# Kernel optimization log

Hardware: AMD Instinct MI355X
Metric: run time of the kernel (lower is better)

## Reference

```python
import jax, jax.numpy as jnp
import numpy as np

HEADS = 8
DIM_HEAD = 64
ROPE_BASE = 10000.0


def _rope_rotate(t):
    """lucidrains-style interleaved RoPE on t: [B, H, N, D]."""
    n, d = t.shape[-2], t.shape[-1]
    inv_freq = 1.0 / (ROPE_BASE ** (jnp.arange(0, d, 2, dtype=jnp.float32) / d))  # [D/2]
    freqs = jnp.arange(n, dtype=jnp.float32)[:, None] * inv_freq[None, :]          # [N, D/2]
    freqs = jnp.repeat(freqs, 2, axis=-1)                                           # [N, D], interleaved
    cos = jnp.cos(freqs).astype(t.dtype)
    sin = jnp.sin(freqs).astype(t.dtype)
    # rotate_half with interleaved pairs: (x1, x2) -> (-x2, x1)
    t2 = t.reshape(t.shape[:-1] + (d // 2, 2))
    rot = jnp.stack([-t2[..., 1], t2[..., 0]], axis=-1).reshape(t.shape)
    return t * cos + rot * sin


def setup_inputs() -> dict:
    key = jax.random.key(0)
    k1, k2, k3, k4 = jax.random.split(key, 4)
    B, N, DIM = 8, 1024, 512
    hidden = HEADS * DIM_HEAD  # 512
    x = jax.random.normal(k1, (B, N, DIM), dtype=jnp.float32)
    pos_bias = jax.random.normal(k2, (HEADS, N, N), dtype=jnp.float32) * 0.1
    w_qkv = jax.random.normal(k3, (DIM, hidden * 3), dtype=jnp.float32) * (DIM ** -0.5)
    w_out = jax.random.normal(k4, (hidden, DIM), dtype=jnp.float32) * (hidden ** -0.5)
    return {"x": x, "pos_bias": pos_bias, "w_qkv": w_qkv, "w_out": w_out}


def reference(x, pos_bias, w_qkv, w_out):
    B, N, _ = x.shape
    qkv = x @ w_qkv                                   # [B, N, 3*H*D]
    q, k, v = jnp.split(qkv, 3, axis=-1)

    def split_heads(t):
        return t.reshape(B, N, HEADS, DIM_HEAD).transpose(0, 2, 1, 3)  # [B, H, N, D]

    q, k, v = map(split_heads, (q, k, v))
    q = q * (DIM_HEAD ** -0.5)
    q = _rope_rotate(q)
    k = _rope_rotate(k)
    sim = jnp.einsum('bhid,bhjd->bhij', q, k) + pos_bias  # pos_bias [H,N,N] broadcasts over B
    attn = jax.nn.softmax(sim, axis=-1)                    # max-subtracted softmax (stable)
    out = jnp.einsum('bhij,bhjd->bhid', attn, v)
    out = out.transpose(0, 2, 1, 3).reshape(B, N, HEADS * DIM_HEAD)
    return out @ w_out
```

## Files before the change

### kernel.cpp

```cpp
#include <hip/hip_runtime.h>

#define DEV __device__ __forceinline__

typedef __attribute__((ext_vector_type(8))) short bf16x8;
typedef __attribute__((ext_vector_type(4))) short bf16x4;
typedef __attribute__((ext_vector_type(4))) float f32x4;
typedef __attribute__((ext_vector_type(4))) unsigned int u32x4;

constexpr int Bb = 8;
constexpr int Nn = 1024;
constexpr int DIMm = 512;
constexpr int Hh = 8;
constexpr int Dh = 64;
constexpr int Mm = Bb * Nn;
constexpr float LN10K = 9.210340371976184f;
constexpr float LOG2E = 1.4426950408889634f;

DEV short f2bf(float f) {
  unsigned int u = __float_as_uint(f);
  u += 0x7fffu + ((u >> 16) & 1u);
  return (short)(u >> 16);
}

DEV unsigned int cvtpk(float lo, float hi) {
  unsigned int r;
  asm("v_cvt_pk_bf16_f32 %0, %1, %2" : "=v"(r) : "v"(lo), "v"(hi));
  return r;
}

DEV bf16x8 comb(bf16x4 lo, bf16x4 hi) {
  bf16x8 r;
  r[0] = lo[0]; r[1] = lo[1]; r[2] = lo[2]; r[3] = lo[3];
  r[4] = hi[0]; r[5] = hi[1]; r[6] = hi[2]; r[7] = hi[3];
  return r;
}

DEV f32x4 mfma16(bf16x8 a, bf16x8 b, f32x4 c) {
  return __builtin_amdgcn_mfma_f32_16x16x32_bf16(a, b, c, 0, 0, 0);
}

DEV void gload16(const void* g, void* l) {
  __builtin_amdgcn_global_load_lds(
      (const __attribute__((address_space(1))) void*)g,
      (__attribute__((address_space(3))) void*)l, 16, 0, 0);
}

__global__ void prep_kernel(const float* __restrict__ x, const float* __restrict__ wq,
                            const float* __restrict__ wo, short* __restrict__ x_bf,
                            short* __restrict__ wqkvT, short* __restrict__ woutT,
                            float2* __restrict__ tab) {
  int stride = gridDim.x * blockDim.x;
  int t = blockIdx.x * blockDim.x + threadIdx.x;
  for (int i = t; i < Mm * DIMm / 4; i += stride) {
    float4 v = ((const float4*)x)[i];
    bf16x4 o;
    o[0] = f2bf(v.x); o[1] = f2bf(v.y); o[2] = f2bf(v.z); o[3] = f2bf(v.w);
    *(bf16x4*)(x_bf + (size_t)i * 4) = o;
  }
  for (int i = t; i < 1536 * 512; i += stride) {
    int n = i >> 9, k = i & 511;
    wqkvT[i] = f2bf(wq[(size_t)k * 1536 + n]);
  }
  for (int i = t; i < 512 * 512; i += stride) {
    int n = i >> 9, k = i & 511;
    woutT[i] = f2bf(wo[(size_t)k * 512 + n]);
  }
  for (int i = t; i < Nn * 32; i += stride) {
    int n = i >> 5, d2 = i & 31;
    float fr = (float)n * __expf(-(float)(2 * d2) * (LN10K / 64.f));
    float sn, cs;
    __sincosf(fr, &sn, &cs);
    tab[i] = make_float2(cs, sn);
  }
}

template <int QKV>
__global__ __launch_bounds__(256) void gemm_k(const short* __restrict__ A,
                                              const short* __restrict__ Bt,
                                              float* __restrict__ outF,
                                              short* __restrict__ qr,
                                              short* __restrict__ kr,
                                              short* __restrict__ vt,
                                              const float2* __restrict__ tab) {
  __shared__ short Al[128][40];
  __shared__ short Bl[128][40];
  const int tid = threadIdx.x;
  const int lane = tid & 63;
  const int wid = tid >> 6;
  const int wm = wid >> 1, wn = wid & 1;
  const int li = lane & 15, g4 = (lane >> 4) << 2;
  const int m0 = blockIdx.x * 128, n0 = blockIdx.y * 128;

  f32x4 zero4 = {0.f, 0.f, 0.f, 0.f};
  f32x4 acc[4][4];
#pragma unroll
  for (int i = 0; i < 4; ++i)
#pragma unroll
    for (int j = 0; j < 4; ++j) acc[i][j] = zero4;

  for (int kt = 0; kt < 512; kt += 32) {
#pragma unroll
    for (int p = 0; p < 2; ++p) {
      int e = (tid + p * 256) * 8;
      int r = e >> 5, c = e & 31;
      *(u32x4*)(&Al[r][c]) = *(const u32x4*)(A + (size_t)(m0 + r) * 512 + kt + c);
      *(u32x4*)(&Bl[r][c]) = *(const u32x4*)(Bt + (size_t)(n0 + r) * 512 + kt + c);
    }
    __syncthreads();
    bf16x8 af[4], bfr[4];
#pragma unroll
    for (int mt = 0; mt < 4; ++mt) {
      int row = wm * 64 + mt * 16 + li;
      af[mt] = comb(*(const bf16x4*)(&Al[row][g4]), *(const bf16x4*)(&Al[row][16 + g4]));
    }
#pragma unroll
    for (int nt = 0; nt < 4; ++nt) {
      int row = wn * 64 + nt * 16 + li;
      bfr[nt] = comb(*(const bf16x4*)(&Bl[row][g4]), *(const bf16x4*)(&Bl[row][16 + g4]));
    }
#pragma unroll
    for (int mt = 0; mt < 4; ++mt)
#pragma unroll
      for (int nt = 0; nt < 4; ++nt)
        acc[mt][nt] = mfma16(af[mt], bfr[nt], acc[mt][nt]);
    __syncthreads();
  }

  if (QKV == 0) {
#pragma unroll
    for (int mt = 0; mt < 4; ++mt) {
      int mb = m0 + wm * 64 + mt * 16 + g4;
#pragma unroll
      for (int nt = 0; nt < 4; ++nt) {
        int c = n0 + wn * 64 + nt * 16 + li;
#pragma unroll
        for (int r = 0; r < 4; ++r) outF[(size_t)(mb + r) * 512 + c] = acc[mt][nt][r];
      }
    }
  } else {
    const int sec = n0 >> 9;
#pragma unroll
    for (int mt = 0; mt < 4; ++mt) {
      int mb = m0 + wm * 64 + mt * 16 + g4;
      int b_ = mb >> 10;
      int nb = mb & 1023;
#pragma unroll
      for (int nt = 0; nt < 4; ++nt) {
        int c = n0 + wn * 64 + nt * 16 + li;
        int cs = c & 511;
        int hh = cs >> 6, d = cs & 63;
        if (sec == 2) {
          uint2 st;
          st.x = cvtpk(acc[mt][nt][0], acc[mt][nt][1]);
          st.y = cvtpk(acc[mt][nt][2], acc[mt][nt][3]);
          *(uint2*)(vt + ((size_t)(b_ * Hh + hh) * Dh + d) * Nn + nb) = st;
        } else {
          short* dst = (sec == 0 ? qr : kr) + ((size_t)(b_ * Hh + hh) * Nn + nb) * Dh + d;
#pragma unroll
          for (int r = 0; r < 4; ++r) {
            float v0 = acc[mt][nt][r];
            float vp = __shfl_xor(v0, 1, 64);
            float2 cssn = tab[(size_t)(nb + r) * 32 + (d >> 1)];
            float rot = (d & 1) ? vp : -vp;
            float res = v0 * cssn.x + rot * cssn.y;
            if (sec == 0) res *= 0.125f * LOG2E;
            dst[(size_t)r * Dh] = f2bf(res);
          }
        }
      }
    }
  }
}

__global__ __launch_bounds__(256, 4) void attn_k(const short* __restrict__ qr,
                                                 const short* __restrict__ kr,
                                                 const short* __restrict__ vt,
                                                 const float* __restrict__ bias,
                                                 short* __restrict__ ao) {
  __shared__ short Kl[128 * 64];
  __shared__ short Vl[64 * 128];
  const int tid = threadIdx.x, lane = tid & 63, w = tid >> 6;
  const int li = lane & 15, g4 = (lane >> 4) << 2;
  const int bid = blockIdx.x;
  const int h = bid & 7;
  const int inner = bid >> 3;
  const int b_ = inner >> 4, it = inner & 15;
  const int bh = b_ * 8 + h;
  const int i0 = it * 64;
  const int iq = i0 + w * 16 + li;

  const short* qrow = qr + ((size_t)bh * Nn + iq) * Dh;
  bf16x8 qf[2];
#pragma unroll
  for (int kk = 0; kk < 2; ++kk)
    qf[kk] = comb(*(const bf16x4*)(qrow + kk * 32 + g4),
                  *(const bf16x4*)(qrow + kk * 32 + 16 + g4));

  const char* KbB = (const char*)(kr + (size_t)bh * Nn * Dh);
  const char* VbB = (const char*)(vt + (size_t)bh * Dh * Nn);
  const float* brow = bias + ((size_t)h * Nn + iq) * Nn;

  float m_run = -1e30f, l_run = 0.f;
  f32x4 zero4 = {0.f, 0.f, 0.f, 0.f};
  f32x4 acc[4];
#pragma unroll
  for (int i = 0; i < 4; ++i) acc[i] = zero4;

  for (int j0 = 0; j0 < Nn; j0 += 128) {
    f32x4 bb[8];
#pragma unroll
    for (int js = 0; js < 8; ++js)
      bb[js] = *(const f32x4*)(brow + j0 + js * 16 + g4);

    __syncthreads();
#pragma unroll
    for (int p = 0; p < 4; ++p) {
      int L = (tid + p * 256) * 16;
      int row = L >> 7, sb = L & 127;
      int gb = sb ^ ((row & 7) << 4);
      gload16(KbB + (size_t)(j0 + row) * 128 + gb, (char*)Kl + L);
      int rv = L >> 8, sv = L & 255;
      int gv = sv ^ ((rv & 7) << 4);
      gload16(VbB + (size_t)rv * 2048 + (size_t)j0 * 2 + gv, (char*)Vl + L);
    }
    __syncthreads();

    f32x4 s[8];
#pragma unroll
    for (int js = 0; js < 8; ++js) {
      int row = js * 16 + li;
      int sw = (row & 7) << 3;
      const short* kb = Kl + row * 64;
      f32x4 sa = bb[js] * LOG2E;
      bf16x8 kf0 = comb(*(const bf16x4*)(kb + ((g4) ^ sw)),
                        *(const bf16x4*)(kb + ((16 + g4) ^ sw)));
      bf16x8 kf1 = comb(*(const bf16x4*)(kb + ((32 + g4) ^ sw)),
                        *(const bf16x4*)(kb + ((48 + g4) ^ sw)));
      sa = mfma16(kf0, qf[0], sa);
      sa = mfma16(kf1, qf[1], sa);
      s[js] = sa;
    }

    float mx = -3e38f;
#pragma unroll
    for (int js = 0; js < 8; ++js) {
      float a = fmaxf(fmaxf(s[js][0], s[js][1]), fmaxf(s[js][2], s[js][3]));
      mx = fmaxf(mx, a);
    }
    mx = fmaxf(mx, __shfl_xor(mx, 16, 64));
    mx = fmaxf(mx, __shfl_xor(mx, 32, 64));

    if (!__all(mx - m_run <= 8.0f)) {
      float mn = fmaxf(m_run, mx);
      float sc = __builtin_amdgcn_exp2f(m_run - mn);
      l_run *= sc;
      m_run = mn;
      float fs0 = __shfl(sc, g4 + 0, 64), fs1 = __shfl(sc, g4 + 1, 64);
      float fs2 = __shfl(sc, g4 + 2, 64), fs3 = __shfl(sc, g4 + 3, 64);
#pragma unroll
      for (int dt = 0; dt < 4; ++dt) {
        acc[dt][0] *= fs0; acc[dt][1] *= fs1;
        acc[dt][2] *= fs2; acc[dt][3] *= fs3;
      }
    }

    float rs = 0.f;
#pragma unroll
    for (int js = 0; js < 8; ++js)
#pragma unroll
      for (int r = 0; r < 4; ++r) {
        float p = __builtin_amdgcn_exp2f(s[js][r] - m_run);
        s[js][r] = p;
        rs += p;
      }
    rs += __shfl_xor(rs, 16, 64);
    rs += __shfl_xor(rs, 32, 64);
    l_run += rs;

    bf16x8 pf[4];
#pragma unroll
    for (int kk = 0; kk < 4; ++kk) {
      union { bf16x8 v; unsigned int d[4]; } u;
      u.d[0] = cvtpk(s[2 * kk][0], s[2 * kk][1]);
      u.d[1] = cvtpk(s[2 * kk][2], s[2 * kk][3]);
      u.d[2] = cvtpk(s[2 * kk + 1][0], s[2 * kk + 1][1]);
      u.d[3] = cvtpk(s[2 * kk + 1][2], s[2 * kk + 1][3]);
      pf[kk] = u.v;
    }

#pragma unroll
    for (int dt = 0; dt < 4; ++dt) {
      int row = dt * 16 + li;
      int sw = (row & 7) << 3;
      const short* vb = Vl + row * 128;
#pragma unroll
      for (int kk = 0; kk < 4; ++kk) {
        int c = kk * 32 + g4;
        bf16x8 vf = comb(*(const bf16x4*)(vb + (c ^ sw)),
                         *(const bf16x4*)(vb + ((c + 16) ^ sw)));
        acc[dt] = mfma16(pf[kk], vf, acc[dt]);
      }
    }
  }

  float rl = 1.f / l_run;
  float fr0 = __shfl(rl, g4 + 0, 64), fr1 = __shfl(rl, g4 + 1, 64);
  float fr2 = __shfl(rl, g4 + 2, 64), fr3 = __shfl(rl, g4 + 3, 64);
#pragma unroll
  for (int dt = 0; dt < 4; ++dt) {
    float fr[4] = {fr0, fr1, fr2, fr3};
#pragma unroll
    for (int r = 0; r < 4; ++r) {
      int i_ = i0 + w * 16 + g4 + r;
      ao[((size_t)(b_ * Nn + i_)) * 512 + h * 64 + dt * 16 + li] =
          f2bf(acc[dt][r] * fr[r]);
    }
  }
}

extern "C" void kernel_launch(void* const* d_in, const int* in_sizes, int n_in,
                              void* d_out, int out_size, void* d_ws, size_t ws_size,
                              hipStream_t stream) {
  const float* x = (const float*)d_in[0];
  const float* pb = (const float*)d_in[1];
  const float* wq = (const float*)d_in[2];
  const float* wo = (const float*)d_in[3];
  float* out = (float*)d_out;

  short* w = (short*)d_ws;
  short* x_bf = w;  w += (size_t)Mm * DIMm;
  short* wqkvT = w; w += 1536 * 512;
  short* woutT = w; w += 512 * 512;
  short* qr = w;    w += (size_t)Mm * DIMm;
  short* kr = w;    w += (size_t)Mm * DIMm;
  short* vt = w;    w += (size_t)Mm * DIMm;
  float2* tab = (float2*)w; w += Nn * 32 * 4;
  short* ao = x_bf;

  prep_kernel<<<1024, 256, 0, stream>>>(x, wq, wo, x_bf, wqkvT, woutT, tab);
  gemm_k<1><<<dim3(64, 12), 256, 0, stream>>>(x_bf, wqkvT, nullptr, qr, kr, vt, tab);
  attn_k<<<1024, 256, 0, stream>>>(qr, kr, vt, pb, ao);
  gemm_k<0><<<dim3(64, 4), 256, 0, stream>>>(ao, woutT, out, nullptr, nullptr, nullptr, tab);
}
```

Measured before the change: 122.4 us.

## Pre-swizzle Q/K/V into MFMA fragment layout and load directly from global

The projection epilogue now writes Q, K and V in a layout where each lane's MFMA fragment is a contiguous 16-byte chunk. The attention kernel then loads K and V fragments straight from global memory into registers instead of staging through LDS with barriers, and processes 64 keys per iteration. It also drops the LOG2E prescale on Q, folding it into the exp2 argument with an FMA, and raises wave priority around MFMA blocks. This removes LDS traffic and __syncthreads, but each wave now fetches K/V independently from global/L2 with no sharing across the block's four waves. Load latency may also be exposed more.

```diff
diff --git a/kernel.cpp b/kernel.cpp
--- a/kernel.cpp
+++ b/kernel.cpp
@@ -37,12 +37,6 @@
 
 DEV f32x4 mfma16(bf16x8 a, bf16x8 b, f32x4 c) {
   return __builtin_amdgcn_mfma_f32_16x16x32_bf16(a, b, c, 0, 0, 0);
-}
-
-DEV void gload16(const void* g, void* l) {
-  __builtin_amdgcn_global_load_lds(
-      (const __attribute__((address_space(1))) void*)g,
-      (__attribute__((address_space(3))) void*)l, 16, 0, 0);
 }
 
 __global__ void prep_kernel(const float* __restrict__ x, const float* __restrict__ wq,
@@ -149,13 +143,25 @@
         int c = n0 + wn * 64 + nt * 16 + li;
         int cs = c & 511;
         int hh = cs >> 6, d = cs & 63;
+        size_t bhoff = (size_t)(b_ * Hh + hh) * 65536;
         if (sec == 2) {
+          int dt = d >> 4, liD = d & 15;
+          int kkJ = (nb >> 5) & 1;
+          int gj = (nb & 15) >> 2;
+          int s0 = (nb & 16) >> 2;
+          size_t off = bhoff + (size_t)(nb >> 6) * 4096 +
+                       (size_t)((dt * 2 + kkJ) * 512) + (size_t)(liD + 16 * gj) * 8 + s0;
           uint2 st;
           st.x = cvtpk(acc[mt][nt][0], acc[mt][nt][1]);
           st.y = cvtpk(acc[mt][nt][2], acc[mt][nt][3]);
-          *(uint2*)(vt + ((size_t)(b_ * Hh + hh) * Dh + d) * Nn + nb) = st;
+          *(uint2*)(vt + off) = st;
         } else {
-          short* dst = (sec == 0 ? qr : kr) + ((size_t)(b_ * Hh + hh) * Nn + nb) * Dh + d;
+          int kkD = d >> 5;
+          int gd = (d & 15) >> 2;
+          int sD = (d & 3) | ((d & 16) >> 2);
+          size_t off = bhoff + (size_t)(nb >> 4) * 1024 + (size_t)(kkD * 512) +
+                       (size_t)((nb & 15) + 16 * gd) * 8 + sD;
+          short* dst = (sec == 0 ? qr : kr) + off;
 #pragma unroll
           for (int r = 0; r < 4; ++r) {
             float v0 = acc[mt][nt][r];
@@ -163,8 +169,8 @@
             float2 cssn = tab[(size_t)(nb + r) * 32 + (d >> 1)];
             float rot = (d & 1) ? vp : -vp;
             float res = v0 * cssn.x + rot * cssn.y;
-            if (sec == 0) res *= 0.125f * LOG2E;
-            dst[(size_t)r * Dh] = f2bf(res);
+            if (sec == 0) res *= 0.125f;
+            dst[(size_t)r * 8] = f2bf(res);
           }
         }
       }
@@ -172,13 +178,11 @@
   }
 }
 
-__global__ __launch_bounds__(256, 4) void attn_k(const short* __restrict__ qr,
-                                                 const short* __restrict__ kr,
-                                                 const short* __restrict__ vt,
+__global__ __launch_bounds__(256, 4) void attn_k(const short* __restrict__ qf_g,
+                                                 const short* __restrict__ kf_g,
+                                                 const short* __restrict__ vf_g,
                                                  const float* __restrict__ bias,
                                                  short* __restrict__ ao) {
-  __shared__ short Kl[128 * 64];
-  __shared__ short Vl[64 * 128];
   const int tid = threadIdx.x, lane = tid & 63, w = tid >> 6;
   const int li = lane & 15, g4 = (lane >> 4) << 2;
   const int bid = blockIdx.x;
@@ -189,16 +193,13 @@
   const int i0 = it * 64;
   const int iq = i0 + w * 16 + li;
 
-  const short* qrow = qr + ((size_t)bh * Nn + iq) * Dh;
-  bf16x8 qf[2];
-#pragma unroll
-  for (int kk = 0; kk < 2; ++kk)
-    qf[kk] = comb(*(const bf16x4*)(qrow + kk * 32 + g4),
-                  *(const bf16x4*)(qrow + kk * 32 + 16 + g4));
-
-  const char* KbB = (const char*)(kr + (size_t)bh * Nn * Dh);
-  const char* VbB = (const char*)(vt + (size_t)bh * Dh * Nn);
-  const float* brow = bias + ((size_t)h * Nn + iq) * Nn;
+  const short* qbase = qf_g + (size_t)bh * 65536 + (size_t)(it * 4 + w) * 1024 + lane * 8;
+  bf16x8 qf0 = *(const bf16x8*)(qbase);
+  bf16x8 qf1 = *(const bf16x8*)(qbase + 512);
+
+  const short* kt = kf_g + (size_t)bh * 65536 + (size_t)lane * 8;
+  const short* vtp = vf_g + (size_t)bh * 65536 + (size_t)lane * 8;
+  const float* brow = bias + ((size_t)h * Nn + iq) * Nn + g4;
 
   float m_run = -1e30f, l_run = 0.f;
   f32x4 zero4 = {0.f, 0.f, 0.f, 0.f};
@@ -206,53 +207,46 @@
 #pragma unroll
   for (int i = 0; i < 4; ++i) acc[i] = zero4;
 
-  for (int j0 = 0; j0 < Nn; j0 += 128) {
-    f32x4 bb[8];
-#pragma unroll
-    for (int js = 0; js < 8; ++js)
-      bb[js] = *(const f32x4*)(brow + j0 + js * 16 + g4);
-
-    __syncthreads();
-#pragma unroll
-    for (int p = 0; p < 4; ++p) {
-      int L = (tid + p * 256) * 16;
-      int row = L >> 7, sb = L & 127;
-      int gb = sb ^ ((row & 7) << 4);
-      gload16(KbB + (size_t)(j0 + row) * 128 + gb, (char*)Kl + L);
-      int rv = L >> 8, sv = L & 255;
-      int gv = sv ^ ((rv & 7) << 4);
-      gload16(VbB + (size_t)rv * 2048 + (size_t)j0 * 2 + gv, (char*)Vl + L);
-    }
-    __syncthreads();
-
-    f32x4 s[8];
-#pragma unroll
-    for (int js = 0; js < 8; ++js) {
-      int row = js * 16 + li;
-      int sw = (row & 7) << 3;
-      const short* kb = Kl + row * 64;
-      f32x4 sa = bb[js] * LOG2E;
-      bf16x8 kf0 = comb(*(const bf16x4*)(kb + ((g4) ^ sw)),
-                        *(const bf16x4*)(kb + ((16 + g4) ^ sw)));
-      bf16x8 kf1 = comb(*(const bf16x4*)(kb + ((32 + g4) ^ sw)),
-                        *(const bf16x4*)(kb + ((48 + g4) ^ sw)));
-      sa = mfma16(kf0, qf[0], sa);
-      sa = mfma16(kf1, qf[1], sa);
-      s[js] = sa;
-    }
-
-    float mx = -3e38f;
-#pragma unroll
-    for (int js = 0; js < 8; ++js) {
-      float a = fmaxf(fmaxf(s[js][0], s[js][1]), fmaxf(s[js][2], s[js][3]));
-      mx = fmaxf(mx, a);
-    }
+  for (int t = 0; t < 16; ++t) {
+    f32x4 bb[4];
+#pragma unroll
+    for (int js = 0; js < 4; ++js) bb[js] = *(const f32x4*)(brow + js * 16);
+    brow += 64;
+
+    bf16x8 kf[8];
+#pragma unroll
+    for (int i = 0; i < 4; ++i) kf[i] = *(const bf16x8*)(kt + i * 512);
+#pragma unroll
+    for (int i = 4; i < 8; ++i) kf[i] = *(const bf16x8*)(kt + 2048 + (i - 4) * 512);
+    kt += 4096;
+
+    f32x4 s[4];
+    __builtin_amdgcn_s_setprio(1);
+#pragma unroll
+    for (int js = 0; js < 4; ++js) {
+      f32x4 sa = mfma16(kf[js * 2], qf0, bb[js]);
+      s[js] = mfma16(kf[js * 2 + 1], qf1, sa);
+    }
+    __builtin_amdgcn_s_setprio(0);
+
+    float mx = fmaxf(fmaxf(fmaxf(s[0][0], s[0][1]), fmaxf(s[0][2], s[0][3])),
+                     fmaxf(fmaxf(s[1][0], s[1][1]), fmaxf(s[1][2], s[1][3])));
+    float mx2 = fmaxf(fmaxf(fmaxf(s[2][0], s[2][1]), fmaxf(s[2][2], s[2][3])),
+                      fmaxf(fmaxf(s[3][0], s[3][1]), fmaxf(s[3][2], s[3][3])));
+    mx = fmaxf(mx, mx2);
     mx = fmaxf(mx, __shfl_xor(mx, 16, 64));
     mx = fmaxf(mx, __shfl_xor(mx, 32, 64));
 
+    bf16x8 vf[8];
+#pragma unroll
+    for (int i = 0; i < 4; ++i) vf[i] = *(const bf16x8*)(vtp + i * 512);
+#pragma unroll
+    for (int i = 4; i < 8; ++i) vf[i] = *(const bf16x8*)(vtp + 2048 + (i - 4) * 512);
+    vtp += 4096;
+
     if (!__all(mx - m_run <= 8.0f)) {
       float mn = fmaxf(m_run, mx);
-      float sc = __builtin_amdgcn_exp2f(m_run - mn);
+      float sc = __builtin_amdgcn_exp2f((m_run - mn) * LOG2E);
       l_run *= sc;
       m_run = mn;
       float fs0 = __shfl(sc, g4 + 0, 64), fs1 = __shfl(sc, g4 + 1, 64);
@@ -264,12 +258,13 @@
       }
     }
 
+    float nm = -m_run * LOG2E;
     float rs = 0.f;
 #pragma unroll
-    for (int js = 0; js < 8; ++js)
+    for (int js = 0; js < 4; ++js)
 #pragma unroll
       for (int r = 0; r < 4; ++r) {
-        float p = __builtin_amdgcn_exp2f(s[js][r] - m_run);
+        float p = __builtin_amdgcn_exp2f(__builtin_fmaf(s[js][r], LOG2E, nm));
         s[js][r] = p;
         rs += p;
       }
@@ -277,9 +272,9 @@
     rs += __shfl_xor(rs, 32, 64);
     l_run += rs;
 
-    bf16x8 pf[4];
-#pragma unroll
-    for (int kk = 0; kk < 4; ++kk) {
+    bf16x8 pf[2];
+#pragma unroll
+    for (int kk = 0; kk < 2; ++kk) {
       union { bf16x8 v; unsigned int d[4]; } u;
       u.d[0] = cvtpk(s[2 * kk][0], s[2 * kk][1]);
       u.d[1] = cvtpk(s[2 * kk][2], s[2 * kk][3]);
@@ -288,19 +283,13 @@
       pf[kk] = u.v;
     }
 
+    __builtin_amdgcn_s_setprio(1);
 #pragma unroll
     for (int dt = 0; dt < 4; ++dt) {
-      int row = dt * 16 + li;
-      int sw = (row & 7) << 3;
-      const short* vb = Vl + row * 128;
-#pragma unroll
-      for (int kk = 0; kk < 4; ++kk) {
-        int c = kk * 32 + g4;
-        bf16x8 vf = comb(*(const bf16x4*)(vb + (c ^ sw)),
-                         *(const bf16x4*)(vb + ((c + 16) ^ sw)));
-        acc[dt] = mfma16(pf[kk], vf, acc[dt]);
-      }
-    }
+      f32x4 a = mfma16(pf[0], vf[dt * 2], acc[dt]);
+      acc[dt] = mfma16(pf[1], vf[dt * 2 + 1], a);
+    }
+    __builtin_amdgcn_s_setprio(0);
   }
 
   float rl = 1.f / l_run;
```

Result: slower. 133.2 us (+8.8%).
